# Kernel optimization log

Measured on AMD Instinct MI355X. Metric: run time of the kernel, lower is better.

The kernel has to match this reference:

```python
import jax, jax.numpy as jnp
import numpy as np

H = 128             # hidden_channels (heads=1 in PyG HGTConv default)
NT, NC, NM = 150000, 40000, 10000   # transactions, customers, merchants
NE = 150000         # edges per base relation
L = 2               # num HGTConv layers
OUT = 2             # out_channels
# node types: 0=transaction, 1=customer, 2=merchant
EDGE_TYPES = ((1, 0), (2, 0), (0, 1), (0, 2))  # (src_type, dst_type)


def setup_inputs():
    key = jax.random.key(0)
    ks = jax.random.split(key, 20)
    s = 1.0 / np.sqrt(H)
    return {
        'x_tx': jax.random.normal(ks[0], (NT, 16), jnp.float32),
        'x_cust': jax.random.normal(ks[1], (NC, 32), jnp.float32),
        'merch_ids': jnp.arange(NM, dtype=jnp.int32),
        'e_ct_src': jax.random.randint(ks[2], (NE,), 0, NC, dtype=jnp.int32),
        'e_ct_dst': jax.random.randint(ks[3], (NE,), 0, NT, dtype=jnp.int32),
        'e_mt_src': jax.random.randint(ks[4], (NE,), 0, NM, dtype=jnp.int32),
        'e_mt_dst': jax.random.randint(ks[5], (NE,), 0, NT, dtype=jnp.int32),
        'proj_tx_w': jax.random.normal(ks[6], (16, H), jnp.float32) * 0.25,
        'proj_tx_b': jnp.zeros((H,), jnp.float32),
        'proj_cust_w': jax.random.normal(ks[7], (32, H), jnp.float32) * 0.18,
        'proj_cust_b': jnp.zeros((H,), jnp.float32),
        'merch_emb': jax.random.normal(ks[8], (NM, H), jnp.float32),
        'kw': jax.random.normal(ks[9], (L, 3, H, H), jnp.float32) * s,
        'kb': jnp.zeros((L, 3, H), jnp.float32),
        'qw': jax.random.normal(ks[10], (L, 3, H, H), jnp.float32) * s,
        'qb': jnp.zeros((L, 3, H), jnp.float32),
        'vw': jax.random.normal(ks[11], (L, 3, H, H), jnp.float32) * s,
        'vb': jnp.zeros((L, 3, H), jnp.float32),
        'aw': jax.random.normal(ks[12], (L, 3, H, H), jnp.float32) * s,
        'ab': jnp.zeros((L, 3, H), jnp.float32),
        'skip': jnp.ones((L, 3), jnp.float32),
        'a_rel': jax.random.normal(ks[13], (L, 4, H, H), jnp.float32) * s,
        'm_rel': jax.random.normal(ks[14], (L, 4, H, H), jnp.float32) * s,
        'p_rel': jnp.ones((L, 4), jnp.float32),
        'out_w': jax.random.normal(ks[15], (H, OUT), jnp.float32) * s,
        'out_b': jnp.zeros((OUT,), jnp.float32),
    }


def _segment_softmax(alpha, dst, n):
    m = jax.ops.segment_max(alpha, dst, num_segments=n)
    m = jnp.where(jnp.isfinite(m), m, 0.0)
    e = jnp.exp(alpha - m[dst])
    z = jax.ops.segment_sum(e, dst, num_segments=n)
    return e / (z[dst] + 1e-16)


def _hgt_conv(xs, lp, edges, sizes):
    kw, kb, qw, qb, vw, vb, aw, ab, skip, a_rel, m_rel, p_rel = lp
    k = [xs[t] @ kw[t] + kb[t] for t in range(3)]
    q = [xs[t] @ qw[t] + qb[t] for t in range(3)]
    v = [xs[t] @ vw[t] + vb[t] for t in range(3)]
    agg = [jnp.zeros_like(xs[t]) for t in range(3)]
    inv_sqrt_d = 1.0 / jnp.sqrt(jnp.float32(H))
    for r, (st, dt) in enumerate(EDGE_TYPES):
        src, dst = edges[r]
        k_e = (k[st] @ a_rel[r])[src]   # [E,H] relation-transformed keys at edge sources
        v_e = (v[st] @ m_rel[r])[src]   # [E,H]
        a = jnp.sum(q[dt][dst] * k_e, axis=-1) * p_rel[r] * inv_sqrt_d  # [E]
        a = _segment_softmax(a, dst, sizes[dt])
        agg[dt] = agg[dt] + jax.ops.segment_sum(a[:, None] * v_e, dst, num_segments=sizes[dt])
    out = []
    for t in range(3):
        o = jax.nn.gelu(agg[t], approximate=False) @ aw[t] + ab[t]
        beta = jax.nn.sigmoid(skip[t])
        out.append(beta * o + (1.0 - beta) * xs[t])
    return out


def _forward(x_tx, x_cust, proj_tx_w, proj_tx_b, proj_cust_w, proj_cust_b, merch_emb,
             kw, kb, qw, qb, vw, vb, aw, ab, skip, a_rel, m_rel, p_rel, out_w, out_b,
             merch_ids, edges):
    xs = [x_tx @ proj_tx_w + proj_tx_b,
          x_cust @ proj_cust_w + proj_cust_b,
          merch_emb[merch_ids]]
    sizes = (NT, NC, NM)
    for l in range(L):
        lp = (kw[l], kb[l], qw[l], qb[l], vw[l], vb[l], aw[l], ab[l], skip[l],
              a_rel[l], m_rel[l], p_rel[l])
        xs = _hgt_conv(xs, lp, edges, sizes)
        xs = [jax.nn.relu(x) for x in xs]   # dropout is identity in eval mode
    return xs[0] @ out_w + out_b            # logits on 'transaction' nodes


def reference(x_tx, x_cust, merch_ids, e_ct_src, e_ct_dst, e_mt_src, e_mt_dst,
              proj_tx_w, proj_tx_b, proj_cust_w, proj_cust_b, merch_emb,
              kw, kb, qw, qb, vw, vb, aw, ab, skip, a_rel, m_rel, p_rel, out_w, out_b):
    edges = ((e_ct_src, e_ct_dst), (e_mt_src, e_mt_dst),
             (e_ct_dst, e_ct_src), (e_mt_dst, e_mt_src))
    return _forward(x_tx, x_cust, proj_tx_w, proj_tx_b, proj_cust_w, proj_cust_b,
                    merch_emb, kw, kb, qw, qb, vw, vb, aw, ab, skip,
                    a_rel, m_rel, p_rel, out_w, out_b, merch_ids, edges)
```

## Files before the change

### kernel.cpp

```cpp
#include <hip/hip_runtime.h>
#include <math.h>

#define H 128
#define NTX 150000
#define NCU 40000
#define NME 10000
#define NEDGE 150000
#define NLAY 2
#define WC_STRIDE 33280
#define WKC_STRIDE 16640
#define EDGEBUF_FLOATS 19200000
#define AGG2_OFF 12800000
#define AGG1_OFF 14080000
#define SCAN_TILE 2048

typedef short s8v __attribute__((ext_vector_type(8)));
typedef float f32x4 __attribute__((ext_vector_type(4)));

__device__ __forceinline__ float gelu_exact(float x) {
    return 0.5f * x * (1.0f + erff(x * 0.70710678118654752f));
}
__device__ __forceinline__ unsigned short f2bf(float x) {
    unsigned u = __float_as_uint(x);
    return (unsigned short)((u + 0x7FFFu + ((u >> 16) & 1u)) >> 16);
}
__device__ __forceinline__ float bf2f(unsigned short b) {
    return __uint_as_float(((unsigned)b) << 16);
}

__global__ __launch_bounds__(256) void fill_val(float* p, int n, float v) {
    int i = blockIdx.x * 256 + threadIdx.x;
    if (i < n) p[i] = v;
}
__global__ __launch_bounds__(256) void zero_int(int* p, int n) {
    int i = blockIdx.x * 256 + threadIdx.x;
    if (i < n) p[i] = 0;
}
__global__ __launch_bounds__(256) void copy_int(int* d, const int* s, int n) {
    int i = blockIdx.x * 256 + threadIdx.x;
    if (i < n) d[i] = s[i];
}

__global__ __launch_bounds__(256) void count_deg(const int* __restrict__ dst,
    int* __restrict__ deg, int E)
{
    int e = blockIdx.x * 256 + threadIdx.x;
    if (e < E) atomicAdd(&deg[dst[e]], 1);
}
__global__ __launch_bounds__(256) void scan1(const int* __restrict__ deg,
    int* __restrict__ out, int* __restrict__ bsum, int n)
{
    __shared__ int ts[256];
    int tid = threadIdx.x;
    int base = blockIdx.x * SCAN_TILE + tid * 8;
    int v[8], pre[8], s = 0;
    #pragma unroll
    for (int j = 0; j < 8; ++j) {
        int idx = base + j;
        v[j] = (idx < n) ? deg[idx] : 0;
        pre[j] = s; s += v[j];
    }
    ts[tid] = s;
    __syncthreads();
    for (int off = 1; off < 256; off <<= 1) {
        int t = (tid >= off) ? ts[tid - off] : 0;
        __syncthreads();
        ts[tid] += t;
        __syncthreads();
    }
    int excl = ts[tid] - s;
    #pragma unroll
    for (int j = 0; j < 8; ++j)
        if (base + j < n) out[base + j] = excl + pre[j];
    if (tid == 255) bsum[blockIdx.x] = ts[255];
}
__global__ __launch_bounds__(64) void scan2(int* __restrict__ bsum, int nb) {
    if (threadIdx.x == 0 && blockIdx.x == 0) {
        int run = 0;
        for (int i = 0; i < nb; ++i) { int t = bsum[i]; bsum[i] = run; run += t; }
    }
}
__global__ __launch_bounds__(256) void scan3(int* __restrict__ out,
    const int* __restrict__ bsum, int n, int total)
{
    int base = blockIdx.x * SCAN_TILE;
    int add = bsum[blockIdx.x];
    for (int j = threadIdx.x; j < SCAN_TILE; j += 256) {
        int k = base + j;
        if (k < n) out[k] += add;
    }
    if (blockIdx.x == 0 && threadIdx.x == 0) out[n] = total;
}
__global__ __launch_bounds__(256) void fill_csr(const int* __restrict__ src,
    const int* __restrict__ dst, int* __restrict__ cursor, int* __restrict__ col, int E)
{
    int e = blockIdx.x * 256 + threadIdx.x;
    if (e >= E) return;
    int pos = atomicAdd(&cursor[dst[e]], 1);
    col[pos] = src[e];
}

template<int K>
__global__ __launch_bounds__(256) void proj_kernel(const float* __restrict__ X,
    const float* __restrict__ W, const float* __restrict__ B,
    float* __restrict__ Y, int N)
{
    int c = threadIdx.x & 127;
    int nl = threadIdx.x >> 7;
    int n = blockIdx.x * 2 + nl;
    if (n >= N) return;
    const float* xr = X + (size_t)n * K;
    float acc = B[c];
    #pragma unroll
    for (int k = 0; k < K; ++k) acc += xr[k] * W[k * H + c];
    Y[(size_t)n * H + c] = acc;
}

__global__ __launch_bounds__(256) void gather_rows(const float* __restrict__ src,
    const int* __restrict__ ids, float* __restrict__ dstp, int N)
{
    int t = blockIdx.x * 256 + threadIdx.x;
    if (t >= N * 32) return;
    int n = t >> 5, c4 = t & 31;
    int sid = ids[n];
    ((float4*)dstp)[(size_t)n * 32 + c4] = ((const float4*)src)[(size_t)sid * 32 + c4];
}

__global__ __launch_bounds__(256) void combine1_par(const float* __restrict__ kw,
    const float* __restrict__ kb, const float* __restrict__ vw, const float* __restrict__ vb,
    const float* __restrict__ a_rel, const float* __restrict__ m_rel,
    float* __restrict__ wkc, float* __restrict__ wc)
{
    __shared__ float Rs[64][132];
    int b = blockIdx.x;
    int combo = b >> 3;
    int pass  = (b >> 2) & 1;
    int slice = b & 3;
    int l = combo >> 2, r = combo & 3;
    const int src_t[4] = {1, 2, 0, 0};
    int st = src_t[r];
    const float* Ap = (pass ? vw : kw) + (size_t)(l*3 + st) * H * H;
    const float* Rp = (pass ? m_rel : a_rel) + (size_t)combo * H * H;
    float* Out = pass ? (wc + (size_t)combo * WC_STRIDE + 16384)
                      : (wkc + (size_t)combo * WKC_STRIDE);

    int tid = threadIdx.x;
    int i = slice * 32 + (tid >> 3);
    int jb = tid & 7;
    float acc[16];
    #pragma unroll
    for (int j = 0; j < 16; ++j) acc[j] = 0.f;

    for (int half = 0; half < 2; ++half) {
        __syncthreads();
        for (int idx = tid; idx < 64 * 128; idx += 256)
            Rs[idx >> 7][idx & 127] = Rp[(half * 64 + (idx >> 7)) * H + (idx & 127)];
        __syncthreads();
        for (int k = 0; k < 64; ++k) {
            float a = Ap[i * H + half * 64 + k];
            #pragma unroll
            for (int j = 0; j < 16; ++j) acc[j] += a * Rs[k][jb + j * 8];
        }
    }
    #pragma unroll
    for (int j = 0; j < 16; ++j) Out[i * H + jb + j * 8] = acc[j];

    if (pass == 0 && slice == 0) {
        const float* Akb = kb + (size_t)(l*3 + st) * H;
        const float* Avb = vb + (size_t)(l*3 + st) * H;
        const float* Rk = a_rel + (size_t)combo * H * H;
        const float* Rv = m_rel + (size_t)combo * H * H;
        float* bkc = wkc + (size_t)combo * WKC_STRIDE + H * H;
        float* bvc = wc + (size_t)combo * WC_STRIDE + 32896;
        if (tid < 128) {
            float s = 0.f;
            for (int k = 0; k < H; ++k) s += Akb[k] * Rk[k * H + tid];
            bkc[tid] = s;
        } else {
            int c = tid - 128;
            float s = 0.f;
            for (int k = 0; k < H; ++k) s += Avb[k] * Rv[k * H + c];
            bvc[c] = s;
        }
    }
}

__global__ __launch_bounds__(256) void combine2_par(const float* __restrict__ qw,
    const float* __restrict__ qb, const float* __restrict__ wkc, float* __restrict__ wc)
{
    __shared__ float BsT[64][133];
    int b = blockIdx.x;
    int combo = b >> 2;
    int slice = b & 3;
    int l = combo >> 2, r = combo & 3;
    const int dst_t[4] = {0, 0, 1, 2};
    int dt = dst_t[r];
    const float* Q  = qw + (size_t)(l*3 + dt) * H * H;
    const float* Qb = qb + (size_t)(l*3 + dt) * H;
    const float* WKc = wkc + (size_t)combo * WKC_STRIDE;
    const float* bkc = WKc + H * H;
    float* QWc = wc + (size_t)combo * WC_STRIDE;

    int tid = threadIdx.x;
    int i = slice * 32 + (tid >> 3);
    int jb = tid & 7;
    float acc[16];
    #pragma unroll
    for (int j = 0; j < 16; ++j) acc[j] = 0.f;

    for (int half = 0; half < 2; ++half) {
        __syncthreads();
        for (int idx = tid; idx < 64 * 128; idx += 256) {
            int j = idx >> 6, k = idx & 63;
            BsT[k][j] = WKc[j * H + half * 64 + k];
        }
        __syncthreads();
        for (int k = 0; k < 64; ++k) {
            float a = Q[i * H + half * 64 + k];
            #pragma unroll
            for (int j = 0; j < 16; ++j) acc[j] += a * BsT[k][jb + j * 8];
        }
    }
    #pragma unroll
    for (int j = 0; j < 16; ++j) QWc[i * H + jb + j * 8] = acc[j];

    if (slice == 0) {
        float* qbc  = wc + (size_t)combo * WC_STRIDE + 32768;
        float* gvec = wc + (size_t)combo * WC_STRIDE + 33024;
        float* gsc  = wc + (size_t)combo * WC_STRIDE + 33152;
        if (tid < 128) {
            float s = 0.f;
            for (int k = 0; k < H; ++k) s += Qb[k] * WKc[tid * H + k];
            qbc[tid] = s;
            if (tid == 0) {
                float g = 0.f;
                for (int k = 0; k < H; ++k) g += Qb[k] * bkc[k];
                gsc[0] = g;
            }
        } else {
            int c = tid - 128;
            float s = 0.f;
            for (int k = 0; k < H; ++k) s += Q[c * H + k] * bkc[k];
            gvec[c] = s;
        }
    }
}

__global__ __launch_bounds__(256) void wprep(const float* __restrict__ wc,
    const float* __restrict__ aw, unsigned short* __restrict__ wt)
{
    int b = blockIdx.x;
    const float* src = (b < 16)
        ? wc + (size_t)(b >> 1) * WC_STRIDE + ((b & 1) ? 16384 : 0)
        : aw + (size_t)(b - 16) * 16384;
    unsigned short* hi = wt + (size_t)b * 32768;
    unsigned short* lo = hi + 16384;
    for (int idx = threadIdx.x; idx < 16384; idx += 256) {
        int k = idx >> 7, j = idx & 127;
        float w = src[idx];
        unsigned short h = f2bf(w);
        hi[j * 128 + k] = h;
        lo[j * 128 + k] = f2bf(w - bf2f(h));
    }
}

template<int MODE, int HASCV>
__global__ __launch_bounds__(256) void mfma_gemm(const float* __restrict__ X,
    const unsigned short* __restrict__ Wt, const float* __restrict__ Bias,
    float* __restrict__ Y, int N, const float* __restrict__ Xold,
    const float* __restrict__ skipP, const float* __restrict__ zb,
    const float* __restrict__ gvecp, const float* __restrict__ gscp,
    float* __restrict__ cvecout)
{
    __shared__ unsigned short lds[2][64][136];
    __shared__ float cacc[64];
    int tid = threadIdx.x;
    int nb = blockIdx.x * 64;

    if (HASCV) {
        if (tid < 64) cacc[tid] = 0.f;
        __syncthreads();
    }

    #pragma unroll
    for (int i = 0; i < 8; ++i) {
        int u = tid + i * 256;
        int n = u >> 5, c4 = u & 31;
        int gn = nb + n;
        float4 v = make_float4(0.f, 0.f, 0.f, 0.f);
        if (gn < N) v = *(const float4*)(X + (size_t)gn * H + c4 * 4);
        if (HASCV) {
            float4 gv = *(const float4*)(gvecp + c4 * 4);
            float part = v.x*gv.x + v.y*gv.y + v.z*gv.z + v.w*gv.w;
            atomicAdd(&cacc[n], part);
        }
        if (MODE == 1) {
            v.x = gelu_exact(v.x); v.y = gelu_exact(v.y);
            v.z = gelu_exact(v.z); v.w = gelu_exact(v.w);
        }
        ushort4 h, lo;
        h.x = f2bf(v.x); lo.x = f2bf(v.x - bf2f(h.x));
        h.y = f2bf(v.y); lo.y = f2bf(v.y - bf2f(h.y));
        h.z = f2bf(v.z); lo.z = f2bf(v.z - bf2f(h.z));
        h.w = f2bf(v.w); lo.w = f2bf(v.w - bf2f(h.w));
        *(ushort4*)&lds[0][n][c4 * 4] = h;
        *(ushort4*)&lds[1][n][c4 * 4] = lo;
    }
    __syncthreads();

    if (HASCV) {
        if (tid < 64 && nb + tid < N) cvecout[nb + tid] = cacc[tid] + gscp[0];
    }

    int wid = tid >> 6, lane = tid & 63;
    int l15 = lane & 15, kg = lane >> 4;
    int col0 = wid * 32;

    s8v bhi[2][4], blo[2][4];
    #pragma unroll
    for (int n = 0; n < 2; ++n) {
        int j = col0 + n * 16 + l15;
        #pragma unroll
        for (int kb = 0; kb < 4; ++kb) {
            bhi[n][kb] = *(const s8v*)(Wt + (size_t)j * 128 + kb * 32 + kg * 8);
            blo[n][kb] = *(const s8v*)(Wt + 16384 + (size_t)j * 128 + kb * 32 + kg * 8);
        }
    }

    f32x4 acc[4][2];
    #pragma unroll
    for (int m = 0; m < 4; ++m)
        #pragma unroll
        for (int n = 0; n < 2; ++n)
            acc[m][n] = (f32x4){0.f, 0.f, 0.f, 0.f};

    #pragma unroll
    for (int m = 0; m < 4; ++m) {
        int row = m * 16 + l15;
        #pragma unroll
        for (int kb = 0; kb < 4; ++kb) {
            s8v ah = *(const s8v*)&lds[0][row][kb * 32 + kg * 8];
            s8v al = *(const s8v*)&lds[1][row][kb * 32 + kg * 8];
            #pragma unroll
            for (int n = 0; n < 2; ++n) {
                acc[m][n] = __builtin_amdgcn_mfma_f32_16x16x32_bf16(ah, bhi[n][kb], acc[m][n], 0, 0, 0);
                acc[m][n] = __builtin_amdgcn_mfma_f32_16x16x32_bf16(al, bhi[n][kb], acc[m][n], 0, 0, 0);
                acc[m][n] = __builtin_amdgcn_mfma_f32_16x16x32_bf16(ah, blo[n][kb], acc[m][n], 0, 0, 0);
            }
        }
    }

    float beta = 0.f, omb = 0.f;
    if (MODE == 1) {
        float s = *skipP;
        beta = 1.f / (1.f + expf(-s));
        omb = 1.f - beta;
    }
    float bias0 = Bias[col0 + l15];
    float bias1 = Bias[col0 + 16 + l15];

    #pragma unroll
    for (int m = 0; m < 4; ++m) {
        #pragma unroll
        for (int r = 0; r < 4; ++r) {
            int grow = nb + m * 16 + kg * 4 + r;
            if (grow < N) {
                float gate = 1.f;
                if (MODE == 2 || MODE == 3) gate = (zb[grow] > 0.f) ? 1.f : 0.f;
                #pragma unroll
                for (int n = 0; n < 2; ++n) {
                    int col = col0 + n * 16 + l15;
                    float val = acc[m][n][r];
                    float bs = n ? bias1 : bias0;
                    size_t yi = (size_t)grow * H + col;
                    if (MODE == 0) {
                        Y[yi] = val + bs;
                    } else if (MODE == 3) {
                        Y[yi] = val + gate * bs;
                    } else if (MODE == 2) {
                        Y[yi] += val + gate * bs;
                    } else {
                        float o = val + bs;
                        float xo = Xold[yi];
                        Y[yi] = fmaxf(beta * o + omb * xo, 0.f);
                    }
                }
            }
        }
    }
}

__global__ __launch_bounds__(256) void gather_agg(const int* __restrict__ row_ptr,
    const int* __restrict__ col_idx, float* __restrict__ qtraw,
    const float* __restrict__ xsrc, const float* __restrict__ cvec,
    const float* __restrict__ prel, int ridx, float* __restrict__ zout, int ndt)
{
    int g = blockIdx.x * 8 + (threadIdx.x >> 5);
    int lane = threadIdx.x & 31;
    if (g >= ndt) return;
    float4 qv = *(const float4*)(qtraw + (size_t)g * H + lane * 4);
    float scale = prel[ridx] * 0.08838834764831843f;
    float cv = cvec[g];
    int beg = row_ptr[g], end = row_ptr[g + 1];
    float4 acc = make_float4(0.f, 0.f, 0.f, 0.f);
    float z = 0.f;
    for (int i = beg; i < end; ++i) {
        int s = col_idx[i];
        float4 xv = *(const float4*)(xsrc + (size_t)s * H + lane * 4);
        float p = qv.x*xv.x + qv.y*xv.y + qv.z*xv.z + qv.w*xv.w;
        #pragma unroll
        for (int m = 16; m >= 1; m >>= 1) p += __shfl_xor(p, m);
        float ev = expf((p + cv) * scale);
        z += ev;
        acc.x += ev * xv.x; acc.y += ev * xv.y;
        acc.z += ev * xv.z; acc.w += ev * xv.w;
    }
    float inv = 1.f / (z + 1e-16f);
    float4 r = make_float4(acc.x * inv, acc.y * inv, acc.z * inv, acc.w * inv);
    *(float4*)(qtraw + (size_t)g * H + lane * 4) = r;
    if (lane == 0) zout[g] = z;
}

__global__ __launch_bounds__(256) void out_kernel(const float* __restrict__ X,
    const float* __restrict__ Wo, const float* __restrict__ bo,
    float* __restrict__ out, int N)
{
    int t = blockIdx.x * 256 + threadIdx.x;
    int n = t >> 5, lane = t & 31;
    if (n >= N) return;
    float4 xv = *(const float4*)(X + (size_t)n * H + lane * 4);
    float xa[4]; *(float4*)xa = xv;
    float p0 = 0.f, p1 = 0.f;
    #pragma unroll
    for (int j = 0; j < 4; ++j) {
        p0 += xa[j] * Wo[(lane*4 + j)*2 + 0];
        p1 += xa[j] * Wo[(lane*4 + j)*2 + 1];
    }
    #pragma unroll
    for (int m = 16; m >= 1; m >>= 1) { p0 += __shfl_xor(p0, m); p1 += __shfl_xor(p1, m); }
    if (lane == 0) {
        out[(size_t)n*2 + 0] = p0 + bo[0];
        out[(size_t)n*2 + 1] = p1 + bo[1];
    }
}

extern "C" void kernel_launch(void* const* d_in, const int* in_sizes, int n_in,
                              void* d_out, int out_size, void* d_ws, size_t ws_size,
                              hipStream_t stream)
{
    const float* x_tx      = (const float*)d_in[0];
    const float* x_cust    = (const float*)d_in[1];
    const int*   merch_ids = (const int*)d_in[2];
    const int*   e_ct_src  = (const int*)d_in[3];
    const int*   e_ct_dst  = (const int*)d_in[4];
    const int*   e_mt_src  = (const int*)d_in[5];
    const int*   e_mt_dst  = (const int*)d_in[6];
    const float* proj_tx_w   = (const float*)d_in[7];
    const float* proj_tx_b   = (const float*)d_in[8];
    const float* proj_cust_w = (const float*)d_in[9];
    const float* proj_cust_b = (const float*)d_in[10];
    const float* merch_emb   = (const float*)d_in[11];
    const float* kw = (const float*)d_in[12];
    const float* kb = (const float*)d_in[13];
    const float* qw = (const float*)d_in[14];
    const float* qb = (const float*)d_in[15];
    const float* vw = (const float*)d_in[16];
    const float* vb = (const float*)d_in[17];
    const float* aw = (const float*)d_in[18];
    const float* ab = (const float*)d_in[19];
    const float* skip  = (const float*)d_in[20];
    const float* a_rel = (const float*)d_in[21];
    const float* m_rel = (const float*)d_in[22];
    const float* p_rel = (const float*)d_in[23];
    const float* out_w = (const float*)d_in[24];
    const float* out_b = (const float*)d_in[25];
    (void)in_sizes; (void)n_in;

    const size_t nsz[3] = {NTX, NCU, NME};

    float* ws = (float*)d_ws;
    size_t off = 0;
    float* xs[3];  for (int t = 0; t < 3; ++t) { xs[t] = ws + off; off += nsz[t]*H; }
    float* agg0    = ws + off; off += (size_t)NTX * H;
    float* edgebuf = ws + off; off += EDGEBUF_FLOATS;
    float* cvec = ws + off; off += NTX;
    float* zbuf = ws + off; off += NTX;
    float* wc   = ws + off; off += 8 * WC_STRIDE;
    float* wkc  = ws + off; off += 8 * WKC_STRIDE;
    int* ibase = (int*)(ws + off);
    const int rp_size[4] = {NTX + 1, NTX + 1, NCU + 1, NME + 1};
    int* rowp[4]; size_t ioff = 0;
    for (int r = 0; r < 4; ++r) { rowp[r] = ibase + ioff; ioff += rp_size[r]; }
    int* colix[4];
    for (int r = 0; r < 4; ++r) { colix[r] = ibase + ioff; ioff += NEDGE; }
    int* cursor = ibase + ioff; ioff += NTX;
    int* bsum   = ibase + ioff; ioff += 256;
    unsigned short* wt = (unsigned short*)(ibase + ioff);
    size_t needed_bytes = off * sizeof(float) + ioff * sizeof(int)
                        + (size_t)22 * 32768 * sizeof(unsigned short);

    float* agg[3] = { agg0, edgebuf + AGG1_OFF, edgebuf + AGG2_OFF };

    if (ws_size < needed_bytes) {
        fill_val<<<(out_size + 255) / 256, 256, 0, stream>>>(
            (float*)d_out, out_size, (float)(ws_size >> 20));
        return;
    }

    const int src_t[4] = {1, 2, 0, 0};
    const int dst_t[4] = {0, 0, 1, 2};
    const int* esrc[4] = {e_ct_src, e_mt_src, e_ct_dst, e_mt_dst};
    const int* edst[4] = {e_ct_dst, e_mt_dst, e_ct_src, e_mt_src};

    const int egrid256 = (NEDGE + 255) / 256;
    for (int r = 0; r < 4; ++r) {
        int ndt = (int)nsz[dst_t[r]];
        int nb = (ndt + SCAN_TILE - 1) / SCAN_TILE;
        zero_int<<<(ndt + 255) / 256, 256, 0, stream>>>(cursor, ndt);
        count_deg<<<egrid256, 256, 0, stream>>>(edst[r], cursor, NEDGE);
        scan1<<<nb, 256, 0, stream>>>(cursor, rowp[r], bsum, ndt);
        scan2<<<1, 64, 0, stream>>>(bsum, nb);
        scan3<<<nb, 256, 0, stream>>>(rowp[r], bsum, ndt, NEDGE);
        copy_int<<<(ndt + 255) / 256, 256, 0, stream>>>(cursor, rowp[r], ndt);
        fill_csr<<<egrid256, 256, 0, stream>>>(esrc[r], edst[r], cursor, colix[r], NEDGE);
    }

    combine1_par<<<64, 256, 0, stream>>>(kw, kb, vw, vb, a_rel, m_rel, wkc, wc);
    combine2_par<<<32, 256, 0, stream>>>(qw, qb, wkc, wc);
    wprep<<<22, 256, 0, stream>>>(wc, aw, wt);

    proj_kernel<16><<<(NTX + 1) / 2, 256, 0, stream>>>(x_tx, proj_tx_w, proj_tx_b, xs[0], NTX);
    proj_kernel<32><<<(NCU + 1) / 2, 256, 0, stream>>>(x_cust, proj_cust_w, proj_cust_b, xs[1], NCU);
    gather_rows<<<(NME * 32 + 255) / 256, 256, 0, stream>>>(merch_emb, merch_ids, xs[2], NME);

    for (int l = 0; l < NLAY; ++l) {
        for (int r = 0; r < 4; ++r) {
            int st = src_t[r], dt = dst_t[r];
            int ndt = (int)nsz[dt];
            int combo = l * 4 + r;
            const float* QWc  = wc + (size_t)combo * WC_STRIDE;
            const float* qbc  = QWc + 32768;
            const float* bvc  = QWc + 32896;
            const float* gvec = QWc + 33024;
            const float* gsc  = QWc + 33152;
            const unsigned short* wtQ = wt + (size_t)(combo * 2 + 0) * 32768;
            const unsigned short* wtV = wt + (size_t)(combo * 2 + 1) * 32768;
            int grid = (ndt + 63) / 64;

            mfma_gemm<0, 1><<<grid, 256, 0, stream>>>(
                xs[dt], wtQ, qbc, edgebuf, ndt, nullptr, nullptr, nullptr,
                gvec, gsc, cvec);
            gather_agg<<<(ndt + 7) / 8, 256, 0, stream>>>(
                rowp[r], colix[r], edgebuf, xs[st], cvec, p_rel, combo, zbuf, ndt);
            if (r == 1)
                mfma_gemm<2, 0><<<grid, 256, 0, stream>>>(
                    edgebuf, wtV, bvc, agg[dt], ndt, nullptr, nullptr, zbuf,
                    nullptr, nullptr, nullptr);
            else
                mfma_gemm<3, 0><<<grid, 256, 0, stream>>>(
                    edgebuf, wtV, bvc, agg[dt], ndt, nullptr, nullptr, zbuf,
                    nullptr, nullptr, nullptr);
        }

        for (int t = 0; t < 3; ++t)
            mfma_gemm<1, 0><<<(int)((nsz[t] + 63) / 64), 256, 0, stream>>>(
                agg[t], wt + (size_t)(16 + l*3 + t) * 32768,
                ab + (size_t)(l*3 + t)*H, xs[t], (int)nsz[t],
                xs[t], skip + l*3 + t, nullptr, nullptr, nullptr, nullptr);
    }

    out_kernel<<<(NTX * 32 + 255) / 256, 256, 0, stream>>>(xs[0], out_w, out_b, (float*)d_out, NTX);
}
```

Before: 1.334 ms.

## Fuse transaction-destination relations into paired Q and V GEMMs, vectorize input projection

The two relations that target transaction nodes now share one Q-side GEMM that stages the transaction tile once and produces both relations' query projections and score vectors. A paired V GEMM sums both aggregated messages in a single accumulator and writes the result once, replacing the read-modify-write accumulate mode. The input projection kernel caches weights in LDS and computes four channels per thread with float4 stores. Workspace buffers are reorganised so the two edge buffers coexist, which uses more memory.

```diff
diff --git a/kernel.cpp b/kernel.cpp
--- a/kernel.cpp
+++ b/kernel.cpp
@@ -9,9 +9,8 @@
 #define NLAY 2
 #define WC_STRIDE 33280
 #define WKC_STRIDE 16640
-#define EDGEBUF_FLOATS 19200000
-#define AGG2_OFF 12800000
-#define AGG1_OFF 14080000
+#define BUF_FLOATS 19200000
+#define AGG2_OFF 5120000
 #define SCAN_TILE 2048
 
 typedef short s8v __attribute__((ext_vector_type(8)));
@@ -105,15 +104,29 @@
     const float* __restrict__ W, const float* __restrict__ B,
     float* __restrict__ Y, int N)
 {
-    int c = threadIdx.x & 127;
-    int nl = threadIdx.x >> 7;
-    int n = blockIdx.x * 2 + nl;
+    __shared__ float Wl[K][128];
+    __shared__ float Bl[128];
+    int tid = threadIdx.x;
+    for (int i = tid; i < K * 128; i += 256) Wl[i >> 7][i & 127] = W[i];
+    if (tid < 128) Bl[tid] = B[tid];
+    __syncthreads();
+    int ng = tid >> 5, lane = tid & 31;
+    int n = blockIdx.x * 8 + ng;
     if (n >= N) return;
     const float* xr = X + (size_t)n * K;
-    float acc = B[c];
-    #pragma unroll
-    for (int k = 0; k < K; ++k) acc += xr[k] * W[k * H + c];
-    Y[(size_t)n * H + c] = acc;
+    float xa[K];
+    #pragma unroll
+    for (int k4 = 0; k4 < K / 4; ++k4)
+        *(float4*)&xa[k4 * 4] = *(const float4*)(xr + k4 * 4);
+    int c0 = lane * 4;
+    float4 acc = *(const float4*)&Bl[c0];
+    #pragma unroll
+    for (int k = 0; k < K; ++k) {
+        float4 w = *(const float4*)&Wl[k][c0];
+        acc.x += xa[k] * w.x; acc.y += xa[k] * w.y;
+        acc.z += xa[k] * w.z; acc.w += xa[k] * w.w;
+    }
+    *(float4*)(Y + (size_t)n * H + c0) = acc;
 }
 
 __global__ __launch_bounds__(256) void gather_rows(const float* __restrict__ src,
@@ -264,6 +277,55 @@
     }
 }
 
+#define STAGE_TILE(SRC, GELU)                                               \
+    _Pragma("unroll")                                                       \
+    for (int i = 0; i < 8; ++i) {                                           \
+        int u = tid + i * 256;                                              \
+        int n = u >> 5, c4 = u & 31;                                        \
+        int gn = nb + n;                                                    \
+        float4 v = make_float4(0.f, 0.f, 0.f, 0.f);                         \
+        if (gn < N) v = *(const float4*)((SRC) + (size_t)gn * H + c4 * 4);  \
+        if (GELU) {                                                         \
+            v.x = gelu_exact(v.x); v.y = gelu_exact(v.y);                   \
+            v.z = gelu_exact(v.z); v.w = gelu_exact(v.w);                   \
+        }                                                                   \
+        ushort4 h, lo;                                                      \
+        h.x = f2bf(v.x); lo.x = f2bf(v.x - bf2f(h.x));                      \
+        h.y = f2bf(v.y); lo.y = f2bf(v.y - bf2f(h.y));                      \
+        h.z = f2bf(v.z); lo.z = f2bf(v.z - bf2f(h.z));                      \
+        h.w = f2bf(v.w); lo.w = f2bf(v.w - bf2f(h.w));                      \
+        *(ushort4*)&lds[0][n][c4 * 4] = h;                                  \
+        *(ushort4*)&lds[1][n][c4 * 4] = lo;                                 \
+    }
+
+#define LOAD_BFRAG(WT)                                                      \
+    _Pragma("unroll")                                                       \
+    for (int n = 0; n < 2; ++n) {                                           \
+        int j = col0 + n * 16 + l15;                                        \
+        _Pragma("unroll")                                                   \
+        for (int kb = 0; kb < 4; ++kb) {                                    \
+            bhi[n][kb] = *(const s8v*)((WT) + (size_t)j * 128 + kb * 32 + kg * 8);          \
+            blo[n][kb] = *(const s8v*)((WT) + 16384 + (size_t)j * 128 + kb * 32 + kg * 8);  \
+        }                                                                   \
+    }
+
+#define MFMA_PASS()                                                         \
+    _Pragma("unroll")                                                       \
+    for (int m = 0; m < 4; ++m) {                                           \
+        int row = m * 16 + l15;                                             \
+        _Pragma("unroll")                                                   \
+        for (int kb = 0; kb < 4; ++kb) {                                    \
+            s8v ah = *(const s8v*)&lds[0][row][kb * 32 + kg * 8];           \
+            s8v al = *(const s8v*)&lds[1][row][kb * 32 + kg * 8];           \
+            _Pragma("unroll")                                               \
+            for (int n = 0; n < 2; ++n) {                                   \
+                acc[m][n] = __builtin_amdgcn_mfma_f32_16x16x32_bf16(ah, bhi[n][kb], acc[m][n], 0, 0, 0); \
+                acc[m][n] = __builtin_amdgcn_mfma_f32_16x16x32_bf16(al, bhi[n][kb], acc[m][n], 0, 0, 0); \
+                acc[m][n] = __builtin_amdgcn_mfma_f32_16x16x32_bf16(ah, blo[n][kb], acc[m][n], 0, 0, 0); \
+            }                                                               \
+        }                                                                   \
+    }
+
 template<int MODE, int HASCV>
 __global__ __launch_bounds__(256) void mfma_gemm(const float* __restrict__ X,
     const unsigned short* __restrict__ Wt, const float* __restrict__ Bias,
@@ -281,33 +343,28 @@
         if (tid < 64) cacc[tid] = 0.f;
         __syncthreads();
     }
-
-    #pragma unroll
-    for (int i = 0; i < 8; ++i) {
-        int u = tid + i * 256;
-        int n = u >> 5, c4 = u & 31;
-        int gn = nb + n;
-        float4 v = make_float4(0.f, 0.f, 0.f, 0.f);
-        if (gn < N) v = *(const float4*)(X + (size_t)gn * H + c4 * 4);
-        if (HASCV) {
+    if (HASCV) {
+        #pragma unroll
+        for (int i = 0; i < 8; ++i) {
+            int u = tid + i * 256;
+            int n = u >> 5, c4 = u & 31;
+            int gn = nb + n;
+            float4 v = make_float4(0.f, 0.f, 0.f, 0.f);
+            if (gn < N) v = *(const float4*)(X + (size_t)gn * H + c4 * 4);
             float4 gv = *(const float4*)(gvecp + c4 * 4);
-            float part = v.x*gv.x + v.y*gv.y + v.z*gv.z + v.w*gv.w;
-            atomicAdd(&cacc[n], part);
-        }
-        if (MODE == 1) {
-            v.x = gelu_exact(v.x); v.y = gelu_exact(v.y);
-            v.z = gelu_exact(v.z); v.w = gelu_exact(v.w);
-        }
-        ushort4 h, lo;
-        h.x = f2bf(v.x); lo.x = f2bf(v.x - bf2f(h.x));
-        h.y = f2bf(v.y); lo.y = f2bf(v.y - bf2f(h.y));
-        h.z = f2bf(v.z); lo.z = f2bf(v.z - bf2f(h.z));
-        h.w = f2bf(v.w); lo.w = f2bf(v.w - bf2f(h.w));
-        *(ushort4*)&lds[0][n][c4 * 4] = h;
-        *(ushort4*)&lds[1][n][c4 * 4] = lo;
+            atomicAdd(&cacc[n], v.x*gv.x + v.y*gv.y + v.z*gv.z + v.w*gv.w);
+            ushort4 h, lo;
+            h.x = f2bf(v.x); lo.x = f2bf(v.x - bf2f(h.x));
+            h.y = f2bf(v.y); lo.y = f2bf(v.y - bf2f(h.y));
+            h.z = f2bf(v.z); lo.z = f2bf(v.z - bf2f(h.z));
+            h.w = f2bf(v.w); lo.w = f2bf(v.w - bf2f(h.w));
+            *(ushort4*)&lds[0][n][c4 * 4] = h;
+            *(ushort4*)&lds[1][n][c4 * 4] = lo;
+        }
+    } else {
+        STAGE_TILE(X, MODE == 1)
     }
     __syncthreads();
-
     if (HASCV) {
         if (tid < 64 && nb + tid < N) cvecout[nb + tid] = cacc[tid] + gscp[0];
     }
@@ -317,15 +374,7 @@
     int col0 = wid * 32;
 
     s8v bhi[2][4], blo[2][4];
-    #pragma unroll
-    for (int n = 0; n < 2; ++n) {
-        int j = col0 + n * 16 + l15;
-        #pragma unroll
-        for (int kb = 0; kb < 4; ++kb) {
-            bhi[n][kb] = *(const s8v*)(Wt + (size_t)j * 128 + kb * 32 + kg * 8);
-            blo[n][kb] = *(const s8v*)(Wt + 16384 + (size_t)j * 128 + kb * 32 + kg * 8);
-        }
-    }
+    LOAD_BFRAG(Wt)
 
     f32x4 acc[4][2];
     #pragma unroll
@@ -334,21 +383,7 @@
         for (int n = 0; n < 2; ++n)
             acc[m][n] = (f32x4){0.f, 0.f, 0.f, 0.f};
 
-    #pragma unroll
-    for (int m = 0; m < 4; ++m) {
-        int row = m * 16 + l15;
-        #pragma unroll
-        for (int kb = 0; kb < 4; ++kb) {
-            s8v ah = *(const s8v*)&lds[0][row][kb * 32 + kg * 8];
-            s8v al = *(const s8v*)&lds[1][row][kb * 32 + kg * 8];
-            #pragma unroll
-            for (int n = 0; n < 2; ++n) {
-                acc[m][n] = __builtin_amdgcn_mfma_f32_16x16x32_bf16(ah, bhi[n][kb], acc[m][n], 0, 0, 0);
-                acc[m][n] = __builtin_amdgcn_mfma_f32_16x16x32_bf16(al, bhi[n][kb], acc[m][n], 0, 0, 0);
-                acc[m][n] = __builtin_amdgcn_mfma_f32_16x16x32_bf16(ah, blo[n][kb], acc[m][n], 0, 0, 0);
-            }
-        }
-    }
+    MFMA_PASS()
 
     float beta = 0.f, omb = 0.f;
     if (MODE == 1) {
@@ -366,7 +401,7 @@
             int grow = nb + m * 16 + kg * 4 + r;
             if (grow < N) {
                 float gate = 1.f;
-                if (MODE == 2 || MODE == 3) gate = (zb[grow] > 0.f) ? 1.f : 0.f;
+                if (MODE == 3) gate = (zb[grow] > 0.f) ? 1.f : 0.f;
                 #pragma unroll
                 for (int n = 0; n < 2; ++n) {
                     int col = col0 + n * 16 + l15;
@@ -377,13 +412,145 @@
                         Y[yi] = val + bs;
                     } else if (MODE == 3) {
                         Y[yi] = val + gate * bs;
-                    } else if (MODE == 2) {
-                        Y[yi] += val + gate * bs;
                     } else {
                         float o = val + bs;
                         float xo = Xold[yi];
                         Y[yi] = fmaxf(beta * o + omb * xo, 0.f);
                     }
+                }
+            }
+        }
+    }
+}
+
+__global__ __launch_bounds__(256) void mfma_gemm2q(const float* __restrict__ X,
+    const unsigned short* __restrict__ Wt0, const unsigned short* __restrict__ Wt1,
+    const float* __restrict__ b0, const float* __restrict__ b1,
+    float* __restrict__ Y0, float* __restrict__ Y1, int N,
+    const float* __restrict__ gv0, const float* __restrict__ gs0, float* __restrict__ cv0,
+    const float* __restrict__ gv1, const float* __restrict__ gs1, float* __restrict__ cv1)
+{
+    __shared__ unsigned short lds[2][64][136];
+    __shared__ float cacc0[64], cacc1[64];
+    int tid = threadIdx.x;
+    int nb = blockIdx.x * 64;
+    if (tid < 64) { cacc0[tid] = 0.f; cacc1[tid] = 0.f; }
+    __syncthreads();
+
+    #pragma unroll
+    for (int i = 0; i < 8; ++i) {
+        int u = tid + i * 256;
+        int n = u >> 5, c4 = u & 31;
+        int gn = nb + n;
+        float4 v = make_float4(0.f, 0.f, 0.f, 0.f);
+        if (gn < N) v = *(const float4*)(X + (size_t)gn * H + c4 * 4);
+        float4 g0 = *(const float4*)(gv0 + c4 * 4);
+        float4 g1 = *(const float4*)(gv1 + c4 * 4);
+        atomicAdd(&cacc0[n], v.x*g0.x + v.y*g0.y + v.z*g0.z + v.w*g0.w);
+        atomicAdd(&cacc1[n], v.x*g1.x + v.y*g1.y + v.z*g1.z + v.w*g1.w);
+        ushort4 h, lo;
+        h.x = f2bf(v.x); lo.x = f2bf(v.x - bf2f(h.x));
+        h.y = f2bf(v.y); lo.y = f2bf(v.y - bf2f(h.y));
+        h.z = f2bf(v.z); lo.z = f2bf(v.z - bf2f(h.z));
+        h.w = f2bf(v.w); lo.w = f2bf(v.w - bf2f(h.w));
+        *(ushort4*)&lds[0][n][c4 * 4] = h;
+        *(ushort4*)&lds[1][n][c4 * 4] = lo;
+    }
+    __syncthreads();
+    if (tid < 64 && nb + tid < N) {
+        cv0[nb + tid] = cacc0[tid] + gs0[0];
+        cv1[nb + tid] = cacc1[tid] + gs1[0];
+    }
+
+    int wid = tid >> 6, lane = tid & 63;
+    int l15 = lane & 15, kg = lane >> 4;
+    int col0 = wid * 32;
+
+    #pragma unroll
+    for (int set = 0; set < 2; ++set) {
+        const unsigned short* Wt = set ? Wt1 : Wt0;
+        const float* Bias = set ? b1 : b0;
+        float* Y = set ? Y1 : Y0;
+
+        s8v bhi[2][4], blo[2][4];
+        LOAD_BFRAG(Wt)
+
+        f32x4 acc[4][2];
+        #pragma unroll
+        for (int m = 0; m < 4; ++m)
+            #pragma unroll
+            for (int n = 0; n < 2; ++n)
+                acc[m][n] = (f32x4){0.f, 0.f, 0.f, 0.f};
+
+        MFMA_PASS()
+
+        float bias0 = Bias[col0 + l15];
+        float bias1 = Bias[col0 + 16 + l15];
+        #pragma unroll
+        for (int m = 0; m < 4; ++m) {
+            #pragma unroll
+            for (int r = 0; r < 4; ++r) {
+                int grow = nb + m * 16 + kg * 4 + r;
+                if (grow < N) {
+                    #pragma unroll
+                    for (int n = 0; n < 2; ++n) {
+                        int col = col0 + n * 16 + l15;
+                        Y[(size_t)grow * H + col] = acc[m][n][r] + (n ? bias1 : bias0);
+                    }
+                }
+            }
+        }
+    }
+}
+
+__global__ __launch_bounds__(256) void mfma_gemmV2(float* __restrict__ A0,
+    const float* __restrict__ A1,
+    const unsigned short* __restrict__ Wt0, const unsigned short* __restrict__ Wt1,
+    const float* __restrict__ bv0, const float* __restrict__ bv1,
+    const float* __restrict__ z0, const float* __restrict__ z1, int N)
+{
+    __shared__ unsigned short lds[2][64][136];
+    int tid = threadIdx.x;
+    int nb = blockIdx.x * 64;
+    int wid = tid >> 6, lane = tid & 63;
+    int l15 = lane & 15, kg = lane >> 4;
+    int col0 = wid * 32;
+
+    f32x4 acc[4][2];
+    #pragma unroll
+    for (int m = 0; m < 4; ++m)
+        #pragma unroll
+        for (int n = 0; n < 2; ++n)
+            acc[m][n] = (f32x4){0.f, 0.f, 0.f, 0.f};
+
+    #pragma unroll
+    for (int half = 0; half < 2; ++half) {
+        const float* A = half ? A1 : A0;
+        const unsigned short* Wt = half ? Wt1 : Wt0;
+        if (half) __syncthreads();
+        STAGE_TILE(A, 0)
+        __syncthreads();
+        s8v bhi[2][4], blo[2][4];
+        LOAD_BFRAG(Wt)
+        MFMA_PASS()
+    }
+
+    float b00 = bv0[col0 + l15],  b01 = bv0[col0 + 16 + l15];
+    float b10 = bv1[col0 + l15],  b11 = bv1[col0 + 16 + l15];
+
+    #pragma unroll
+    for (int m = 0; m < 4; ++m) {
+        #pragma unroll
+        for (int r = 0; r < 4; ++r) {
+            int grow = nb + m * 16 + kg * 4 + r;
+            if (grow < N) {
+                float g0 = (z0[grow] > 0.f) ? 1.f : 0.f;
+                float g1 = (z1[grow] > 0.f) ? 1.f : 0.f;
+                #pragma unroll
+                for (int n = 0; n < 2; ++n) {
+                    int col = col0 + n * 16 + l15;
+                    float bs = n ? (g0 * b01 + g1 * b11) : (g0 * b00 + g1 * b10);
+                    A0[(size_t)grow * H + col] = acc[m][n][r] + bs;
                 }
             }
         }
@@ -481,10 +648,12 @@
     float* ws = (float*)d_ws;
     size_t off = 0;
     float* xs[3];  for (int t = 0; t < 3; ++t) { xs[t] = ws + off; off += nsz[t]*H; }
-    float* agg0    = ws + off; off += (size_t)NTX * H;
-    float* edgebuf = ws + off; off += EDGEBUF_FLOATS;
-    float* cvec = ws + off; off += NTX;
-    float* zbuf = ws + off; off += NTX;
+    float* bufB    = ws + off; off += BUF_FLOATS;
+    float* edgebuf = ws + off; off += BUF_FLOATS;
+    float* cvec0 = ws + off; off += NTX;
+    float* cvec1 = ws + off; off += NTX;
+    float* zbuf0 = ws + off; off += NTX;
+    float* zbuf1 = ws + off; off += NTX;
     float* wc   = ws + off; off += 8 * WC_STRIDE;
     float* wkc  = ws + off; off += 8 * WKC_STRIDE;
     int* ibase = (int*)(ws + off);
@@ -499,8 +668,6 @@
     size_t needed_bytes = off * sizeof(float) + ioff * sizeof(int)
                         + (size_t)22 * 32768 * sizeof(unsigned short);
 
-    float* agg[3] = { agg0, edgebuf + AGG1_OFF, edgebuf + AGG2_OFF };
-
     if (ws_size < needed_bytes) {
         fill_val<<<(out_size + 255) / 256, 256, 0, stream>>>(
             (float*)d_out, out_size, (float)(ws_size >> 20));
@@ -529,42 +696,49 @@
     combine2_par<<<32, 256, 0, stream>>>(qw, qb, wkc, wc);
     wprep<<<22, 256, 0, stream>>>(wc, aw, wt);
 
-    proj_kernel<16><<<(NTX + 1) / 2, 256, 0, stream>>>(x_tx, proj_tx_w, proj_tx_b, xs[0], NTX);
-    proj_kernel<32><<<(NCU + 1) / 2, 256, 0, stream>>>(x_cust, proj_cust_w, proj_cust_b, xs[1], NCU);
+    proj_kernel<16><<<(NTX + 7) / 8, 256, 0, stream>>>(x_tx, proj_tx_w, proj_tx_b, xs[0], NTX);
+    proj_kernel<32><<<(NCU + 7) / 8, 256, 0, stream>>>(x_cust, proj_cust_w, proj_cust_b, xs[1], NCU);
     gather_rows<<<(NME * 32 + 255) / 256, 256, 0, stream>>>(merch_emb, merch_ids, xs[2], NME);
 
+    float* aggT[3] = { edgebuf, bufB, bufB + AGG2_OFF };
+
     for (int l = 0; l < NLAY; ++l) {
-        for (int r = 0; r < 4; ++r) {
+        int c0 = l * 4 + 0, c1 = l * 4 + 1;
+        const float* W0 = wc + (size_t)c0 * WC_STRIDE;
+        const float* W1 = wc + (size_t)c1 * WC_STRIDE;
+
+        mfma_gemm2q<<<(NTX + 63) / 64, 256, 0, stream>>>(
+            xs[0], wt + (size_t)(c0*2) * 32768, wt + (size_t)(c1*2) * 32768,
+            W0 + 32768, W1 + 32768, edgebuf, bufB, NTX,
+            W0 + 33024, W0 + 33152, cvec0, W1 + 33024, W1 + 33152, cvec1);
+        gather_agg<<<(NTX + 7) / 8, 256, 0, stream>>>(
+            rowp[0], colix[0], edgebuf, xs[1], cvec0, p_rel, c0, zbuf0, NTX);
+        gather_agg<<<(NTX + 7) / 8, 256, 0, stream>>>(
+            rowp[1], colix[1], bufB, xs[2], cvec1, p_rel, c1, zbuf1, NTX);
+        mfma_gemmV2<<<(NTX + 63) / 64, 256, 0, stream>>>(
+            edgebuf, bufB, wt + (size_t)(c0*2 + 1) * 32768, wt + (size_t)(c1*2 + 1) * 32768,
+            W0 + 32896, W1 + 32896, zbuf0, zbuf1, NTX);
+
+        for (int r = 2; r < 4; ++r) {
             int st = src_t[r], dt = dst_t[r];
             int ndt = (int)nsz[dt];
             int combo = l * 4 + r;
-            const float* QWc  = wc + (size_t)combo * WC_STRIDE;
-            const float* qbc  = QWc + 32768;
-            const float* bvc  = QWc + 32896;
-            const float* gvec = QWc + 33024;
-            const float* gsc  = QWc + 33152;
-            const unsigned short* wtQ = wt + (size_t)(combo * 2 + 0) * 32768;
-            const unsigned short* wtV = wt + (size_t)(combo * 2 + 1) * 32768;
+            const float* Wr = wc + (size_t)combo * WC_STRIDE;
+            float* buf = aggT[dt];
             int grid = (ndt + 63) / 64;
-
             mfma_gemm<0, 1><<<grid, 256, 0, stream>>>(
-                xs[dt], wtQ, qbc, edgebuf, ndt, nullptr, nullptr, nullptr,
-                gvec, gsc, cvec);
+                xs[dt], wt + (size_t)(combo*2) * 32768, Wr + 32768, buf, ndt,
+                nullptr, nullptr, nullptr, Wr + 33024, Wr + 33152, cvec0);
             gather_agg<<<(ndt + 7) / 8, 256, 0, stream>>>(
-                rowp[r], colix[r], edgebuf, xs[st], cvec, p_rel, combo, zbuf, ndt);
-            if (r == 1)
-                mfma_gemm<2, 0><<<grid, 256, 0, stream>>>(
-                    edgebuf, wtV, bvc, agg[dt], ndt, nullptr, nullptr, zbuf,
-                    nullptr, nullptr, nullptr);
-            else
-                mfma_gemm<3, 0><<<grid, 256, 0, stream>>>(
-                    edgebuf, wtV, bvc, agg[dt], ndt, nullptr, nullptr, zbuf,
-                    nullptr, nullptr, nullptr);
+                rowp[r], colix[r], buf, xs[st], cvec0, p_rel, combo, zbuf0, ndt);
+            mfma_gemm<3, 0><<<grid, 256, 0, stream>>>(
+                buf, wt + (size_t)(combo*2 + 1) * 32768, Wr + 32896, buf, ndt,
+                nullptr, nullptr, zbuf0, nullptr, nullptr, nullptr);
         }
 
         for (int t = 0; t < 3; ++t)
             mfma_gemm<1, 0><<<(int)((nsz[t] + 63) / 64), 256, 0, stream>>>(
-                agg[t], wt + (size_t)(16 + l*3 + t) * 32768,
+                aggT[t], wt + (size_t)(16 + l*3 + t) * 32768,
                 ab + (size_t)(l*3 + t)*H, xs[t], (int)nsz[t],
                 xs[t], skip + l*3 + t, nullptr, nullptr, nullptr, nullptr);
     }
```

New measurement: 1.236 ms. 7.3% less time.
